# Kernel optimization log

Measured on AMD Instinct MI355X. Metric: run time of the kernel, lower is better.

## Reference

```python
import jax, jax.numpy as jnp
import numpy as np

B, S, IN_DIM, OUT_DIM, DV = 64, 8192, 512, 128, 128


def setup_inputs() -> dict:
    key = jax.random.key(0)
    k1, k2, k3, k4, k5 = jax.random.split(key, 5)
    # xavier_uniform bound = sqrt(6/(fan_in+fan_out))
    bk = float(np.sqrt(6.0 / (OUT_DIM + OUT_DIM)))
    bq = float(np.sqrt(6.0 / (IN_DIM + OUT_DIM)))
    return {
        "k": jax.random.normal(k1, (B, S, OUT_DIM), dtype=jnp.float32),
        "q": jax.random.normal(k2, (B, IN_DIM), dtype=jnp.float32),
        "v": jax.random.normal(k3, (B, S, DV), dtype=jnp.float32),
        "Wk": jax.random.uniform(k4, (OUT_DIM, OUT_DIM), jnp.float32, -bk, bk),
        "Wq": jax.random.uniform(k5, (IN_DIM, OUT_DIM), jnp.float32, -bq, bq),
    }


def reference(k, q, v, Wk, Wq):
    scale = jnp.sqrt(jnp.asarray(OUT_DIM, dtype=k.dtype))
    key = jnp.einsum("bsd,de->bse", k, Wk)          # [B,S,out_dim]
    query = q @ Wq                                     # [B,out_dim]
    score = jnp.einsum("be,bse->bs", query, key) / scale  # [B,S]
    attn = jax.nn.softmax(score, axis=-1)              # [B,S]
    context = jnp.einsum("bs,bsv->bv", attn, v)       # [B,dv]
    return context
```

## Files before the change

### kernel.cpp

```cpp
#include <hip/hip_runtime.h>
#include <math.h>

#define BB 64
#define SS 8192
#define IN_DIM 512
#define OUT_DIM 128
#define DVV 128
#define CHUNK 256
#define NCHUNK (SS / CHUNK)

__global__ __launch_bounds__(512) void qt_kernel(const float* __restrict__ q,
                          const float* __restrict__ Wq,
                          const float* __restrict__ Wk,
                          float* __restrict__ qt) {
    int b = blockIdx.x;
    int t = threadIdx.x;
    int e = t & 127;
    int h = t >> 7;
    __shared__ float part[4][OUT_DIM];
    __shared__ float qs[OUT_DIM];

    const float* qb = q + (size_t)b * IN_DIM;
    float acc = 0.f;
    for (int i = h * (IN_DIM / 4); i < (h + 1) * (IN_DIM / 4); ++i)
        acc = fmaf(qb[i], Wq[(size_t)i * OUT_DIM + e], acc);
    part[h][e] = acc;
    __syncthreads();
    if (h == 0) qs[e] = part[0][e] + part[1][e] + part[2][e] + part[3][e];
    __syncthreads();

    float a2 = 0.f;
    const float* wkrow = Wk + (size_t)e * OUT_DIM;
    for (int i = h * (OUT_DIM / 4); i < (h + 1) * (OUT_DIM / 4); ++i)
        a2 = fmaf(wkrow[i], qs[i], a2);
    part[h][e] = a2;
    __syncthreads();
    if (h == 0)
        qt[(size_t)b * OUT_DIM + e] =
            (part[0][e] + part[1][e] + part[2][e] + part[3][e]) * 0.08838834764831845f;
}

__global__ __launch_bounds__(256) void partial_kernel(
    const float* __restrict__ k, const float* __restrict__ v,
    const float* __restrict__ qt, float* __restrict__ ml,
    float* __restrict__ ctx) {
    int blk = blockIdx.x;
    int b = blk / NCHUNK;
    int c = blk % NCHUNK;
    int s0 = c * CHUNK;
    int t = threadIdx.x;
    int g = t >> 5;
    int l32 = t & 31;

    __shared__ float4 qts4[OUT_DIM / 4];
    __shared__ float gm[8], gl[8];
    __shared__ float4 gacc[8][32];

    if (t < OUT_DIM / 4)
        qts4[t] = ((const float4*)(qt + (size_t)b * OUT_DIM))[t];
    __syncthreads();
    float4 qv = qts4[l32];

    const float4* k4 = (const float4*)(k + (size_t)b * SS * OUT_DIM);
    const float4* v4 = (const float4*)(v + (size_t)b * SS * DVV);

    float m = -INFINITY, l = 0.f;
    float4 acc = make_float4(0.f, 0.f, 0.f, 0.f);

    #pragma unroll 4
    for (int j = 0; j < CHUNK / 8; ++j) {
        int i = s0 + g + 8 * j;
        float4 kv = k4[(size_t)i * (OUT_DIM / 4) + l32];
        float4 vv = v4[(size_t)i * (DVV / 4) + l32];
        float p = kv.x * qv.x + kv.y * qv.y + kv.z * qv.z + kv.w * qv.w;
        p += __shfl_xor(p, 1);
        p += __shfl_xor(p, 2);
        p += __shfl_xor(p, 4);
        p += __shfl_xor(p, 8);
        p += __shfl_xor(p, 16);
        float mnew = fmaxf(m, p);
        float cr = __expf(m - mnew);
        float e = __expf(p - mnew);
        l = l * cr + e;
        acc.x = fmaf(acc.x, cr, e * vv.x);
        acc.y = fmaf(acc.y, cr, e * vv.y);
        acc.z = fmaf(acc.z, cr, e * vv.z);
        acc.w = fmaf(acc.w, cr, e * vv.w);
        m = mnew;
    }

    if (l32 == 0) gm[g] = m;
    __syncthreads();
    float M = gm[0];
    #pragma unroll
    for (int i = 1; i < 8; ++i) M = fmaxf(M, gm[i]);
    float scale = __expf(m - M);
    if (l32 == 0) gl[g] = l * scale;
    float4 sa;
    sa.x = acc.x * scale; sa.y = acc.y * scale;
    sa.z = acc.z * scale; sa.w = acc.w * scale;
    gacc[g][l32] = sa;
    __syncthreads();

    if (t < 32) {
        float4 r = gacc[0][t];
        #pragma unroll
        for (int i2 = 1; i2 < 8; ++i2) {
            float4 o = gacc[i2][t];
            r.x += o.x; r.y += o.y; r.z += o.z; r.w += o.w;
        }
        ((float4*)(ctx + ((size_t)(b * NCHUNK + c)) * DVV))[t] = r;
    }
    if (t == 0) {
        float L = gl[0];
        #pragma unroll
        for (int i3 = 1; i3 < 8; ++i3) L += gl[i3];
        ml[(b * NCHUNK + c) * 2 + 0] = M;
        ml[(b * NCHUNK + c) * 2 + 1] = L;
    }
}

__global__ void combine_kernel(const float* __restrict__ ml,
                               const float* __restrict__ ctx,
                               float* __restrict__ out) {
    int b = blockIdx.x;
    int t = threadIdx.x;
    __shared__ float ms, ls;
    float m = -INFINITY;
    if (t < NCHUNK) m = ml[(b * NCHUNK + t) * 2];
    for (int d = 1; d < 32; d <<= 1) m = fmaxf(m, __shfl_xor(m, d));
    if (t == 0) ms = m;
    __syncthreads();
    m = ms;
    float l = 0.f;
    if (t < NCHUNK)
        l = ml[(b * NCHUNK + t) * 2 + 1] * __expf(ml[(b * NCHUNK + t) * 2] - m);
    for (int d = 1; d < 32; d <<= 1) l += __shfl_xor(l, d);
    if (t == 0) ls = l;
    __syncthreads();
    l = ls;
    float acc = 0.f;
    for (int c2 = 0; c2 < NCHUNK; ++c2) {
        float w = __expf(ml[(b * NCHUNK + c2) * 2] - m);
        acc = fmaf(ctx[((size_t)(b * NCHUNK + c2)) * DVV + t], w, acc);
    }
    out[(size_t)b * DVV + t] = acc / l;
}

extern "C" void kernel_launch(void* const* d_in, const int* in_sizes, int n_in,
                              void* d_out, int out_size, void* d_ws, size_t ws_size,
                              hipStream_t stream) {
    const float* k  = (const float*)d_in[0];
    const float* q  = (const float*)d_in[1];
    const float* v  = (const float*)d_in[2];
    const float* Wk = (const float*)d_in[3];
    const float* Wq = (const float*)d_in[4];
    float* out = (float*)d_out;

    float* qt  = (float*)d_ws;
    float* ml  = qt + BB * OUT_DIM;
    float* ctx = ml + BB * NCHUNK * 2;

    qt_kernel<<<BB, 512, 0, stream>>>(q, Wq, Wk, qt);
    partial_kernel<<<BB * NCHUNK, 256, 0, stream>>>(k, v, qt, ml, ctx);
    combine_kernel<<<BB, DVV, 0, stream>>>(ml, ctx, out);
}
```

Measured before the change: 147.4 us.

## Use two-pass softmax per warp and emit per-warp partials to combine kernel

Each 32-lane group now loads all its K rows first, computes scores into registers and the row max, and only then streams V with exp weights. This replaces the serial online-softmax rescaling, whose exp chain depends on the previous iteration, and it allows many independent K loads in flight. The in-block shared-memory reduction and barriers are removed, and each warp writes its own partial (m, l, ctx), which makes the partial buffer 8x larger. The combine kernel now merges 256 partials per batch through shared memory. The cost is more register pressure from the 32-entry score array and more workspace traffic.

After: 169.4 us. 1.15x slower.

```diff
diff --git a/kernel.cpp b/kernel.cpp
--- a/kernel.cpp
+++ b/kernel.cpp
@@ -8,6 +8,9 @@
 #define DVV 128
 #define CHUNK 256
 #define NCHUNK (SS / CHUNK)
+#define NGRP 8
+#define RPG (CHUNK / NGRP)
+#define NPART (NCHUNK * NGRP)
 
 __global__ __launch_bounds__(512) void qt_kernel(const float* __restrict__ q,
                           const float* __restrict__ Wq,
@@ -45,106 +48,84 @@
     const float* __restrict__ qt, float* __restrict__ ml,
     float* __restrict__ ctx) {
     int blk = blockIdx.x;
-    int b = blk / NCHUNK;
-    int c = blk % NCHUNK;
+    int b = blk >> 5;
+    int c = blk & 31;
     int s0 = c * CHUNK;
     int t = threadIdx.x;
     int g = t >> 5;
     int l32 = t & 31;
 
-    __shared__ float4 qts4[OUT_DIM / 4];
-    __shared__ float gm[8], gl[8];
-    __shared__ float4 gacc[8][32];
+    float4 qv = ((const float4*)(qt + (size_t)b * OUT_DIM))[l32];
 
-    if (t < OUT_DIM / 4)
-        qts4[t] = ((const float4*)(qt + (size_t)b * OUT_DIM))[t];
-    __syncthreads();
-    float4 qv = qts4[l32];
+    const float4* k4 = (const float4*)(k + (size_t)b * SS * OUT_DIM)
+                       + (size_t)(s0 + g) * (OUT_DIM / 4) + l32;
+    const float4* v4 = (const float4*)(v + (size_t)b * SS * DVV)
+                       + (size_t)(s0 + g) * (DVV / 4) + l32;
 
-    const float4* k4 = (const float4*)(k + (size_t)b * SS * OUT_DIM);
-    const float4* v4 = (const float4*)(v + (size_t)b * SS * DVV);
-
-    float m = -INFINITY, l = 0.f;
-    float4 acc = make_float4(0.f, 0.f, 0.f, 0.f);
-
-    #pragma unroll 4
-    for (int j = 0; j < CHUNK / 8; ++j) {
-        int i = s0 + g + 8 * j;
-        float4 kv = k4[(size_t)i * (OUT_DIM / 4) + l32];
-        float4 vv = v4[(size_t)i * (DVV / 4) + l32];
+    float s[RPG];
+    float m = -INFINITY;
+    #pragma unroll
+    for (int j = 0; j < RPG; ++j) {
+        float4 kv = k4[j * 8 * (OUT_DIM / 4)];
         float p = kv.x * qv.x + kv.y * qv.y + kv.z * qv.z + kv.w * qv.w;
         p += __shfl_xor(p, 1);
         p += __shfl_xor(p, 2);
         p += __shfl_xor(p, 4);
         p += __shfl_xor(p, 8);
         p += __shfl_xor(p, 16);
-        float mnew = fmaxf(m, p);
-        float cr = __expf(m - mnew);
-        float e = __expf(p - mnew);
-        l = l * cr + e;
-        acc.x = fmaf(acc.x, cr, e * vv.x);
-        acc.y = fmaf(acc.y, cr, e * vv.y);
-        acc.z = fmaf(acc.z, cr, e * vv.z);
-        acc.w = fmaf(acc.w, cr, e * vv.w);
-        m = mnew;
+        s[j] = p;
+        m = fmaxf(m, p);
     }
 
-    if (l32 == 0) gm[g] = m;
-    __syncthreads();
-    float M = gm[0];
+    float l = 0.f;
+    float4 acc = make_float4(0.f, 0.f, 0.f, 0.f);
     #pragma unroll
-    for (int i = 1; i < 8; ++i) M = fmaxf(M, gm[i]);
-    float scale = __expf(m - M);
-    if (l32 == 0) gl[g] = l * scale;
-    float4 sa;
-    sa.x = acc.x * scale; sa.y = acc.y * scale;
-    sa.z = acc.z * scale; sa.w = acc.w * scale;
-    gacc[g][l32] = sa;
-    __syncthreads();
+    for (int j = 0; j < RPG; ++j) {
+        float4 vv = v4[j * 8 * (DVV / 4)];
+        float w = __expf(s[j] - m);
+        l += w;
+        acc.x = fmaf(w, vv.x, acc.x);
+        acc.y = fmaf(w, vv.y, acc.y);
+        acc.z = fmaf(w, vv.z, acc.z);
+        acc.w = fmaf(w, vv.w, acc.w);
+    }
 
-    if (t < 32) {
-        float4 r = gacc[0][t];
-        #pragma unroll
-        for (int i2 = 1; i2 < 8; ++i2) {
-            float4 o = gacc[i2][t];
-            r.x += o.x; r.y += o.y; r.z += o.z; r.w += o.w;
-        }
-        ((float4*)(ctx + ((size_t)(b * NCHUNK + c)) * DVV))[t] = r;
-    }
-    if (t == 0) {
-        float L = gl[0];
-        #pragma unroll
-        for (int i3 = 1; i3 < 8; ++i3) L += gl[i3];
-        ml[(b * NCHUNK + c) * 2 + 0] = M;
-        ml[(b * NCHUNK + c) * 2 + 1] = L;
+    size_t gi = (size_t)blk * NGRP + g;
+    ((float4*)(ctx + gi * DVV))[l32] = acc;
+    if (l32 == 0) {
+        ml[gi * 2 + 0] = m;
+        ml[gi * 2 + 1] = l;
     }
 }
 
-__global__ void combine_kernel(const float* __restrict__ ml,
-                               const float* __restrict__ ctx,
-                               float* __restrict__ out) {
+__global__ __launch_bounds__(256) void combine_kernel(
+    const float* __restrict__ ml, const float* __restrict__ ctx,
+    float* __restrict__ out) {
     int b = blockIdx.x;
     int t = threadIdx.x;
-    __shared__ float ms, ls;
-    float m = -INFINITY;
-    if (t < NCHUNK) m = ml[(b * NCHUNK + t) * 2];
-    for (int d = 1; d < 32; d <<= 1) m = fmaxf(m, __shfl_xor(m, d));
-    if (t == 0) ms = m;
+    __shared__ float sm[NPART], sl[NPART], sw[NPART];
+
+    sm[t] = ml[((size_t)b * NPART + t) * 2 + 0];
+    sl[t] = ml[((size_t)b * NPART + t) * 2 + 1];
     __syncthreads();
-    m = ms;
-    float l = 0.f;
-    if (t < NCHUNK)
-        l = ml[(b * NCHUNK + t) * 2 + 1] * __expf(ml[(b * NCHUNK + t) * 2] - m);
-    for (int d = 1; d < 32; d <<= 1) l += __shfl_xor(l, d);
-    if (t == 0) ls = l;
+
+    float M = -INFINITY;
+    #pragma unroll 8
+    for (int i = 0; i < NPART; ++i) M = fmaxf(M, sm[i]);
+    sw[t] = __expf(sm[t] - M);
     __syncthreads();
-    l = ls;
-    float acc = 0.f;
-    for (int c2 = 0; c2 < NCHUNK; ++c2) {
-        float w = __expf(ml[(b * NCHUNK + c2) * 2] - m);
-        acc = fmaf(ctx[((size_t)(b * NCHUNK + c2)) * DVV + t], w, acc);
+
+    if (t < DVV) {
+        float L = 0.f;
+        #pragma unroll 8
+        for (int i = 0; i < NPART; ++i) L = fmaf(sl[i], sw[i], L);
+        float acc = 0.f;
+        const float* cb = ctx + (size_t)b * NPART * DVV + t;
+        #pragma unroll 8
+        for (int i = 0; i < NPART; ++i)
+            acc = fmaf(sw[i], cb[(size_t)i * DVV], acc);
+        out[(size_t)b * DVV + t] = acc / L;
     }
-    out[(size_t)b * DVV + t] = acc / l;
 }
 
 extern "C" void kernel_launch(void* const* d_in, const int* in_sizes, int n_in,
@@ -159,9 +140,9 @@
 
     float* qt  = (float*)d_ws;
     float* ml  = qt + BB * OUT_DIM;
-    float* ctx = ml + BB * NCHUNK * 2;
+    float* ctx = ml + (size_t)BB * NPART * 2;
 
     qt_kernel<<<BB, 512, 0, stream>>>(q, Wq, Wk, qt);
     partial_kernel<<<BB * NCHUNK, 256, 0, stream>>>(k, v, qt, ml, ctx);
-    combine_kernel<<<BB, DVV, 0, stream>>>(ml, ctx, out);
+    combine_kernel<<<BB, 256, 0, stream>>>(ml, ctx, out);
 }
```
